# Performance work log

Hardware: AMD Instinct MI355X
Metric: run time of the kernel (lower is better)

The kernel has to match this reference:

```python
import jax, jax.numpy as jnp
import numpy as np
import math

D = 2048
NH = 16       # query heads
NKV = 4       # kv heads (GQA)
HD = 128
SOFTCLAMP = 50.0
ROPE_BASE = 10000.0
B = 4
SQ_VLM = 1024
SQ_ACT = 64
S_CACHE = 256


def _heads(x, n):
    # [B,S,n*HD] -> [B,n,S,HD]
    b, s, _ = x.shape
    return x.reshape(b, s, n, HD).transpose(0, 2, 1, 3)


def _rope_cos_sin(pos):
    # pos: [B,S] int -> cos,sin [B,1,S,HD]
    inv_freq = 1.0 / (ROPE_BASE ** (jnp.arange(0, HD, 2, dtype=jnp.float32) / HD))
    freqs = pos.astype(jnp.float32)[..., None] * inv_freq  # [B,S,HD/2]
    emb = jnp.concatenate([freqs, freqs], axis=-1)         # [B,S,HD]
    return jnp.cos(emb)[:, None], jnp.sin(emb)[:, None]


def _apply_rope(x, cos, sin):
    # x: [B,H,S,HD]
    x1, x2 = x[..., : HD // 2], x[..., HD // 2 :]
    rot = jnp.concatenate([-x2, x1], axis=-1)
    return x * cos + rot * sin


def setup_inputs() -> dict:
    key = jax.random.key(0)
    ks = jax.random.split(key, 16)
    sc = lambda d: 1.0 / math.sqrt(d)
    inp = {
        'attention_mask': jnp.zeros((B, 1, SQ_VLM + SQ_ACT, S_CACHE + SQ_VLM + SQ_ACT), jnp.float32),
        'pos_vlm': jnp.broadcast_to(jnp.arange(S_CACHE, S_CACHE + SQ_VLM, dtype=jnp.int32), (B, SQ_VLM)),
        'pos_action': jnp.broadcast_to(jnp.arange(S_CACHE + SQ_VLM, S_CACHE + SQ_VLM + SQ_ACT, dtype=jnp.int32), (B, SQ_ACT)),
        'h_vlm': jax.random.normal(ks[0], (B, SQ_VLM, D), jnp.float32),
        'h_action': jax.random.normal(ks[1], (B, SQ_ACT, D), jnp.float32),
        'k_cache': jax.random.normal(ks[2], (B, NKV, S_CACHE, HD), jnp.float32),
        'v_cache': jax.random.normal(ks[3], (B, NKV, S_CACHE, HD), jnp.float32),
        'Wq_vlm': jax.random.normal(ks[4], (D, NH * HD), jnp.float32) * sc(D),
        'Wk_vlm': jax.random.normal(ks[5], (D, NKV * HD), jnp.float32) * sc(D),
        'Wv_vlm': jax.random.normal(ks[6], (D, NKV * HD), jnp.float32) * sc(D),
        'Wq_act': jax.random.normal(ks[7], (D, NH * HD), jnp.float32) * sc(D),
        'Wk_act': jax.random.normal(ks[8], (D, NKV * HD), jnp.float32) * sc(D),
        'Wv_act': jax.random.normal(ks[9], (D, NKV * HD), jnp.float32) * sc(D),
        'Wo_act': jax.random.normal(ks[10], (NH * HD, D), jnp.float32) * sc(NH * HD),
    }
    return inp


def reference(attention_mask, pos_vlm, pos_action, h_vlm, h_action, k_cache, v_cache,
              Wq_vlm, Wk_vlm, Wv_vlm, Wq_act, Wk_act, Wv_act, Wo_act):
    group = NH // NKV

    def qkv(h, pos, Wq, Wk, Wv):
        q = _heads(h @ Wq, NH)
        k = _heads(h @ Wk, NKV)
        v = _heads(h @ Wv, NKV)
        cos, sin = _rope_cos_sin(pos)
        return _apply_rope(q, cos, sin), _apply_rope(k, cos, sin), v

    q_v, k_v, v_v = qkv(h_vlm, pos_vlm, Wq_vlm, Wk_vlm, Wv_vlm)
    q_a, k_a, v_a = qkv(h_action, pos_action, Wq_act, Wk_act, Wv_act)

    # repeat_kv (GQA) on every KV source, cached mixture first (append_non_active order)
    rep = lambda t: jnp.repeat(t, group, axis=1)  # [B,NKV,S,HD] -> [B,NH,S,HD]
    k = jnp.concatenate([rep(k_cache), rep(k_v), rep(k_a)], axis=2)
    v = jnp.concatenate([rep(v_cache), rep(v_v), rep(v_a)], axis=2)
    q = jnp.concatenate([q_v, q_a], axis=2)  # [B,NH,Sq,HD]

    scores = jnp.einsum('bhqd,bhkd->bhqk', q, k) / math.sqrt(HD)
    scores = jnp.tanh(scores / SOFTCLAMP) * SOFTCLAMP + attention_mask
    w = jax.nn.softmax(scores.astype(jnp.float32), axis=-1).astype(q.dtype)
    out = jnp.einsum('bhqk,bhkd->bhqd', w, v)
    out = out.transpose(0, 2, 1, 3).reshape(B, SQ_VLM + SQ_ACT, NH * HD)

    # split by q_lens; 'vlm' is in post_attn_skip_names -> no o_proj, dropped
    out_action = out[:, SQ_VLM:, :]
    return out_action @ Wo_act
```

## Files before the change

kernel.cpp:

```cpp
#include <hip/hip_runtime.h>
#include <cmath>

#define NH 16
#define NKV 4
#define HD 128
#define DMODEL 2048
#define BB 4
#define SQV 1024
#define SQA 64
#define SCACHE 256
#define STOT 1344
#define SQTOT 1088
#define NSPLIT 7

typedef unsigned short u16;
typedef __attribute__((ext_vector_type(8))) short short8;
typedef __attribute__((ext_vector_type(4))) float f32x4;

__device__ __forceinline__ float b2f(u16 u) {
    union { float f; unsigned int i; } x; x.i = ((unsigned int)u) << 16; return x.f;
}
__device__ __forceinline__ u16 f2b(float f) {
    unsigned int x = __float_as_uint(f);
    x = x + 0x7fffu + ((x >> 16) & 1u);
    return (u16)(x >> 16);
}

__device__ __forceinline__ void gload16(const void* g, void* l) {
    __builtin_amdgcn_global_load_lds((const __attribute__((address_space(1))) void*)g,
                                     (__attribute__((address_space(3))) void*)l, 16, 0, 0);
}

__device__ __forceinline__ void transpose_body(const float* in, u16* out, int N,
                                               int bx, int by) {
    __shared__ __align__(16) u16 t[64 * 66];
    int n0 = bx * 64, k0 = by * 64;
    int tid = threadIdx.x;
    int r = tid >> 3;
    int c8 = (tid & 7) * 8;
#pragma unroll
    for (int h = 0; h < 2; h++) {
        int k = r + h * 32;
        const float* f = in + (size_t)(k0 + k) * N + n0 + c8;
        float4 a = *(const float4*)f, b = *(const float4*)(f + 4);
        u16 vv[8] = {f2b(a.x), f2b(a.y), f2b(a.z), f2b(a.w),
                     f2b(b.x), f2b(b.y), f2b(b.z), f2b(b.w)};
#pragma unroll
        for (int j = 0; j < 8; j++) t[(c8 + j) * 66 + k] = vv[j];
    }
    __syncthreads();
#pragma unroll
    for (int h = 0; h < 2; h++) {
        int n = r + h * 32;
        short8 v;
#pragma unroll
        for (int j = 0; j < 8; j++) ((u16*)&v)[j] = t[n * 66 + c8 + j];
        *(short8*)(out + (size_t)(n0 + n) * 2048 + k0 + c8) = v;
    }
}

__global__ void k_prep(const float* __restrict__ mask,
                       const float* __restrict__ kc, const float* __restrict__ vc,
                       const float* __restrict__ hv, const float* __restrict__ ha,
                       const float* __restrict__ w0, u16* __restrict__ o0,
                       const float* __restrict__ w1, u16* __restrict__ o1,
                       const float* __restrict__ w2, u16* __restrict__ o2,
                       const float* __restrict__ w3, u16* __restrict__ o3,
                       const float* __restrict__ w4, u16* __restrict__ o4,
                       const float* __restrict__ w5, u16* __restrict__ o5,
                       float* __restrict__ cosT, float* __restrict__ sinT,
                       u16* __restrict__ maskS, u16* __restrict__ K_all, u16* __restrict__ V_all,
                       u16* __restrict__ hv16, u16* __restrict__ ha16) {
    int gx = blockIdx.x, tid = threadIdx.x;
    if (gx < 3072) {
        if (gx < 256)        transpose_body(w0, o0, 512,  gx & 7,  gx >> 3);
        else if (gx < 512)   { int g = gx - 256;  transpose_body(w1, o1, 512,  g & 7,  g >> 3); }
        else if (gx < 768)   { int g = gx - 512;  transpose_body(w2, o2, 512,  g & 7,  g >> 3); }
        else if (gx < 1024)  { int g = gx - 768;  transpose_body(w3, o3, 512,  g & 7,  g >> 3); }
        else if (gx < 2048)  { int g = gx - 1024; transpose_body(w4, o4, 2048, g & 31, g >> 5); }
        else                 { int g = gx - 2048; transpose_body(w5, o5, 2048, g & 31, g >> 5); }
        return;
    }
    int bx = gx - 3072;
    if (bx < 336) {
        int i = bx * 256 + tid;
        if (i < STOT * 64) {
            int p = i >> 6, j = i & 63;
            float inv = __expf(-(float)j * (9.210340371976184f / 64.0f));
            float ang = (float)p * inv;
            cosT[i] = cosf(ang);
            sinT[i] = sinf(ang);
        }
    } else if (bx < 1680) {
        int i = (bx - 336) * 256 + tid;
        int b = i / (SQA * STOT);
        int r = i % (SQA * STOT);
        size_t s = (size_t)b * SQTOT * STOT + (size_t)SQV * STOT + r;
        maskS[i] = f2b(mask[s]);
    } else if (bx < 1936) {
        int i = (bx - 1680) * 256 + tid;
        int e = i * 8;
        int bk = e / (SCACHE * HD);
        int off = e % (SCACHE * HD);
        size_t dst = (size_t)bk * STOT * HD + off;
        const float* fk = kc + e;
        const float* fv = vc + e;
        u16 tk[8], tv[8];
#pragma unroll
        for (int j = 0; j < 8; j++) { tk[j] = f2b(fk[j]); tv[j] = f2b(fv[j]); }
        *(short8*)(K_all + dst) = *(short8*)tk;
        *(short8*)(V_all + dst) = *(short8*)tv;
    } else if (bx < 6032) {
        int i = (bx - 1936) * 256 + tid;
        int e = i * 8;
        const float* f = hv + e;
        float4 a = *(const float4*)f, b = *(const float4*)(f + 4);
        u16 t[8] = {f2b(a.x), f2b(a.y), f2b(a.z), f2b(a.w),
                    f2b(b.x), f2b(b.y), f2b(b.z), f2b(b.w)};
        *(short8*)(hv16 + e) = *(short8*)t;
    } else {
        int i = (bx - 6032) * 256 + tid;
        int e = i * 8;
        const float* f = ha + e;
        float4 a = *(const float4*)f, b = *(const float4*)(f + 4);
        u16 t[8] = {f2b(a.x), f2b(a.y), f2b(a.z), f2b(a.w),
                    f2b(b.x), f2b(b.y), f2b(b.z), f2b(b.w)};
        *(short8*)(ha16 + e) = *(short8*)t;
    }
}

__global__ __launch_bounds__(256) void k_gemm_qkv(
    const u16* __restrict__ Avlm, const u16* __restrict__ Aact,
    const u16* __restrict__ WkvT, const u16* __restrict__ WvvT,
    const u16* __restrict__ WqaT, const u16* __restrict__ WkaT, const u16* __restrict__ WvaT,
    const int* __restrict__ pos_vlm, const int* __restrict__ pos_act,
    const float* __restrict__ cosT, const float* __restrict__ sinT,
    u16* __restrict__ Qbuf, u16* __restrict__ K_all, u16* __restrict__ V_all) {
    __shared__ __align__(16) u16 smem[2 * 12288];
    int tid = threadIdx.x;
    int w = tid >> 6, lane = tid & 63;
    int la = lane & 15, lg = lane >> 4;
    int wm = (w & 1) * 32;
    int c2 = w >> 1;
    int ntab[4] = {c2 * 2, c2 * 2 + 1, c2 * 2 + 4, c2 * 2 + 5};

    const u16* A; const u16* Bt; int m0, n0;
    int path;
    int kv_or_head = 0;
    if (blockIdx.y < 8) {
        int by = blockIdx.y;
        m0 = blockIdx.x * 64;
        A = Avlm;
        path = (by < 4) ? 0 : 1;
        kv_or_head = by & 3;
        n0 = kv_or_head * 128;
        Bt = (path == 0) ? WkvT : WvvT;
    } else {
        int g = (blockIdx.y - 8) * 64 + blockIdx.x;
        if (g >= 96) return;
        m0 = (g & 3) * 64;
        int ny = g >> 2;
        A = Aact;
        if (ny < 16)      { path = 2; kv_or_head = ny;      Bt = WqaT; n0 = ny * 128; }
        else if (ny < 20) { path = 3; kv_or_head = ny - 16; Bt = WkaT; n0 = (ny - 16) * 128; }
        else              { path = 4; kv_or_head = ny - 20; Bt = WvaT; n0 = (ny - 20) * 128; }
    }

    f32x4 acc[2][4];
#pragma unroll
    for (int i = 0; i < 2; i++)
#pragma unroll
        for (int j = 0; j < 4; j++) acc[i][j] = (f32x4){0.f, 0.f, 0.f, 0.f};

    int srow = tid >> 3;
    int scsrc = (((tid & 7) * 16) ^ ((srow & 7) << 4)) >> 1;

#define STAGE_QKV(CB, KB) do {                                                        \
        u16* Ab_ = smem + (CB) * 12288;                                               \
        u16* Bb_ = Ab_ + 4096;                                                        \
        _Pragma("unroll")                                                             \
        for (int h = 0; h < 2; h++)                                                   \
            gload16(A + (size_t)(m0 + srow + h * 32) * DMODEL + (KB) + scsrc,         \
                    Ab_ + h * 2048 + w * 512);                                        \
        _Pragma("unroll")                                                             \
        for (int h = 0; h < 4; h++)                                                   \
            gload16(Bt + (size_t)(n0 + srow + h * 32) * DMODEL + (KB) + scsrc,        \
                    Bb_ + h * 2048 + w * 512);                                        \
    } while (0)

    STAGE_QKV(0, 0);
    int cur = 0;
    int sw = (la & 7) << 3;
    for (int kb = 0; kb < DMODEL; kb += 64) {
        if (kb + 64 < DMODEL) {
            STAGE_QKV(cur ^ 1, kb + 64);
            asm volatile("s_waitcnt vmcnt(6)" ::: "memory");
        } else {
            asm volatile("s_waitcnt vmcnt(0)" ::: "memory");
        }
        __builtin_amdgcn_s_barrier();
        asm volatile("" ::: "memory");
        const u16* Ac = smem + cur * 12288;
        const u16* Bc = Ac + 4096;
#pragma unroll
        for (int kk = 0; kk < 2; kk++) {
            short8 af[2], bf[4];
            int cc = (kk * 32 + lg * 8) ^ sw;
#pragma unroll
            for (int mt = 0; mt < 2; mt++)
                af[mt] = *(const short8*)&Ac[(wm + mt * 16 + la) * 64 + cc];
#pragma unroll
            for (int nt = 0; nt < 4; nt++)
                bf[nt] = *(const short8*)&Bc[(ntab[nt] * 16 + la) * 64 + cc];
#pragma unroll
            for (int mt = 0; mt < 2; mt++)
#pragma unroll
                for (int nt = 0; nt < 4; nt++)
                    acc[mt][nt] = __builtin_amdgcn_mfma_f32_16x16x32_bf16(af[mt], bf[nt], acc[mt][nt], 0, 0, 0);
        }
        __builtin_amdgcn_s_barrier();
        cur ^= 1;
    }
#undef STAGE_QKV

#pragma unroll
    for (int mt = 0; mt < 2; mt++) {
#pragma unroll
        for (int r = 0; r < 4; r++) {
            int gm = m0 + wm + mt * 16 + lg * 4 + r;
            if (path <= 1) {
                int b = gm >> 10, s = gm & 1023;
                size_t base = ((size_t)(b * NKV + kv_or_head) * STOT + SCACHE + s) * HD;
                if (path == 0) {
                    int pos = pos_vlm[gm];
#pragma unroll
                    for (int i = 0; i < 2; i++) {
                        int dlo = ntab[i] * 16 + la;
                        float x1 = acc[mt][i][r], x2 = acc[mt][i + 2][r];
                        float cs = cosT[pos * 64 + dlo], sn = sinT[pos * 64 + dlo];
                        K_all[base + dlo]      = f2b(x1 * cs - x2 * sn);
                        K_all[base + dlo + 64] = f2b(x2 * cs + x1 * sn);
                    }
                } else {
#pragma unroll
                    for (int i = 0; i < 4; i++) V_all[base + ntab[i] * 16 + la] = f2b(acc[mt][i][r]);
                }
            } else {
                int b = gm >> 6, s = gm & 63;
                if (path == 2) {
                    int pos = pos_act[gm];
                    size_t qb = ((size_t)(b * NH + kv_or_head) * SQA + s) * HD;
#pragma unroll
                    for (int i = 0; i < 2; i++) {
                        int dlo = ntab[i] * 16 + la;
                        float x1 = acc[mt][i][r], x2 = acc[mt][i + 2][r];
                        float cs = cosT[pos * 64 + dlo], sn = sinT[pos * 64 + dlo];
                        Qbuf[qb + dlo]      = f2b(x1 * cs - x2 * sn);
                        Qbuf[qb + dlo + 64] = f2b(x2 * cs + x1 * sn);
                    }
                } else if (path == 3) {
                    int pos = pos_act[gm];
                    size_t base = ((size_t)(b * NKV + kv_or_head) * STOT + SCACHE + SQV + s) * HD;
#pragma unroll
                    for (int i = 0; i < 2; i++) {
                        int dlo = ntab[i] * 16 + la;
                        float x1 = acc[mt][i][r], x2 = acc[mt][i + 2][r];
                        float cs = cosT[pos * 64 + dlo], sn = sinT[pos * 64 + dlo];
                        K_all[base + dlo]      = f2b(x1 * cs - x2 * sn);
                        K_all[base + dlo + 64] = f2b(x2 * cs + x1 * sn);
                    }
                } else {
                    size_t base = ((size_t)(b * NKV + kv_or_head) * STOT + SCACHE + SQV + s) * HD;
#pragma unroll
                    for (int i = 0; i < 4; i++) V_all[base + ntab[i] * 16 + la] = f2b(acc[mt][i][r]);
                }
            }
        }
    }
}

__global__ __launch_bounds__(256) void k_attn_split(
    const u16* __restrict__ Qbuf, const u16* __restrict__ K_all, const u16* __restrict__ V_all,
    const u16* __restrict__ maskS, u16* __restrict__ po, float* __restrict__ pml) {
    int h = blockIdx.x, b = blockIdx.y, p = blockIdx.z;
    int bh = b * NH + h;
    int kvh = h >> 2;
    const u16* Kb = K_all + (size_t)(b * NKV + kvh) * STOT * HD;
    const u16* Vb = V_all + (size_t)(b * NKV + kvh) * STOT * HD;
    const u16* Qb = Qbuf + (size_t)bh * SQA * HD;
    int tid = threadIdx.x, w = tid >> 6, lane = tid & 63;
    int la = lane & 15, lg = lane >> 4;
    __shared__ __align__(16) u16 Ks[64 * 136];
    __shared__ __align__(16) u16 Vs[64 * 130];
    __shared__ __align__(16) u16 Ps[4][16 * 72];
    short8 qf[4];
#pragma unroll
    for (int kk = 0; kk < 4; kk++)
        qf[kk] = *(const short8*)(Qb + (size_t)(w * 16 + la) * HD + kk * 32 + lg * 8);
    f32x4 o_acc[8];
#pragma unroll
    for (int nt = 0; nt < 8; nt++) o_acc[nt] = (f32x4){0.f, 0.f, 0.f, 0.f};
    float m_run[4], l_run[4];
#pragma unroll
    for (int r = 0; r < 4; r++) { m_run[r] = -3e38f; l_run[r] = 0.f; }
    int vr = tid >> 4;
    int vc = (tid & 15) * 8;
    const float scl = 0.08838834764831845f;
    for (int c = 0; c < 3; c++) {
        int g = p * 3 + c;
#pragma unroll
        for (int hh = 0; hh < 4; hh++) {
            int key = vr + hh * 16;
            *(short8*)&Ks[key * 136 + vc] = *(const short8*)(Kb + (size_t)(g * 64 + key) * HD + vc);
            short8 vv = *(const short8*)(Vb + (size_t)(g * 64 + key) * HD + vc);
            unsigned int* d32 = (unsigned int*)&Vs[key * 130 + vc];
#pragma unroll
            for (int q2 = 0; q2 < 4; q2++) d32[q2] = ((unsigned int*)&vv)[q2];
        }
        __syncthreads();
        f32x4 s_acc[4];
#pragma unroll
        for (int nt = 0; nt < 4; nt++) s_acc[nt] = (f32x4){0.f, 0.f, 0.f, 0.f};
#pragma unroll
        for (int kk = 0; kk < 4; kk++) {
#pragma unroll
            for (int nt = 0; nt < 4; nt++) {
                short8 kf = *(const short8*)&Ks[(nt * 16 + la) * 136 + kk * 32 + lg * 8];
                s_acc[nt] = __builtin_amdgcn_mfma_f32_16x16x32_bf16(qf[kk], kf, s_acc[nt], 0, 0, 0);
            }
        }
        float sc[4][4];
#pragma unroll
        for (int nt = 0; nt < 4; nt++) {
            int key = g * 64 + nt * 16 + la;
#pragma unroll
            for (int r = 0; r < 4; r++) {
                int sq = w * 16 + lg * 4 + r;
                float sv = s_acc[nt][r] * scl;
                float x = sv * 0.02f;
                float t = __expf(-2.0f * fabsf(x));
                float th = __fdividef(1.0f - t, 1.0f + t);
                sv = copysignf(th, x) * 50.0f;
                sv += b2f(maskS[((size_t)(b * SQA + sq)) * STOT + key]);
                sc[nt][r] = sv;
            }
        }
#pragma unroll
        for (int r = 0; r < 4; r++) {
            float mx = fmaxf(fmaxf(sc[0][r], sc[1][r]), fmaxf(sc[2][r], sc[3][r]));
#pragma unroll
            for (int sh = 1; sh < 16; sh <<= 1) mx = fmaxf(mx, __shfl_xor(mx, sh, 64));
            float mn = fmaxf(m_run[r], mx);
            float alpha = __expf(m_run[r] - mn);
            m_run[r] = mn;
            float rowsum = 0.f;
#pragma unroll
            for (int nt = 0; nt < 4; nt++) {
                float pv = __expf(sc[nt][r] - mn);
                Ps[w][(lg * 4 + r) * 72 + nt * 16 + la] = f2b(pv);
                rowsum += pv;
            }
#pragma unroll
            for (int sh = 1; sh < 16; sh <<= 1) rowsum += __shfl_xor(rowsum, sh, 64);
            l_run[r] = l_run[r] * alpha + rowsum;
#pragma unroll
            for (int nt = 0; nt < 8; nt++) o_acc[nt][r] *= alpha;
        }
        __syncthreads();
#pragma unroll
        for (int kk = 0; kk < 2; kk++) {
            short8 pf = *(const short8*)&Ps[w][la * 72 + kk * 32 + lg * 8];
#pragma unroll
            for (int nt = 0; nt < 8; nt++) {
                short8 vf;
#pragma unroll
                for (int j = 0; j < 8; j++) ((u16*)&vf)[j] = Vs[(kk * 32 + lg * 8 + j) * 130 + nt * 16 + la];
                o_acc[nt] = __builtin_amdgcn_mfma_f32_16x16x32_bf16(pf, vf, o_acc[nt], 0, 0, 0);
            }
        }
        __syncthreads();
    }
#pragma unroll
    for (int nt = 0; nt < 8; nt++) {
#pragma unroll
        for (int r = 0; r < 4; r++) {
            int sq = w * 16 + lg * 4 + r;
            po[(((size_t)p * 64 + bh) * 64 + sq) * 128 + nt * 16 + la] = f2b(o_acc[nt][r]);
        }
    }
    if (la == 0) {
#pragma unroll
        for (int r = 0; r < 4; r++) {
            int sq = w * 16 + lg * 4 + r;
            size_t mlb = (((size_t)p * 64 + bh) * 64 + sq) * 2;
            pml[mlb] = m_run[r];
            pml[mlb + 1] = l_run[r];
        }
    }
}

__global__ __launch_bounds__(256) void k_attn_red(
    const u16* __restrict__ po, const float* __restrict__ pml, u16* __restrict__ AO) {
    int h = blockIdx.x, b = blockIdx.y;
    int bh = b * NH + h;
    __shared__ float wgt[NSPLIT][64];
    int tid = threadIdx.x;
    if (tid < 64) {
        int q = tid;
        float m[NSPLIT], l[NSPLIT], M = -3e38f;
#pragma unroll
        for (int p = 0; p < NSPLIT; p++) {
            size_t mlb = (((size_t)p * 64 + bh) * 64 + q) * 2;
            m[p] = pml[mlb]; l[p] = pml[mlb + 1];
            M = fmaxf(M, m[p]);
        }
        float L = 0.f;
#pragma unroll
        for (int p = 0; p < NSPLIT; p++) L += l[p] * __expf(m[p] - M);
        float inv = 1.0f / L;
#pragma unroll
        for (int p = 0; p < NSPLIT; p++) wgt[p][q] = __expf(m[p] - M) * inv;
    }
    __syncthreads();
    for (int e = tid; e < 64 * 128; e += 256) {
        int q = e >> 7, d = e & 127;
        float s = 0.f;
#pragma unroll
        for (int p = 0; p < NSPLIT; p++)
            s += b2f(po[(((size_t)p * 64 + bh) * 64 + q) * 128 + d]) * wgt[p][q];
        AO[((size_t)(b * SQA + q)) * 2048 + h * HD + d] = f2b(s);
    }
}

__global__ __launch_bounds__(256) void k_gemm_out(
    const u16* __restrict__ A, const u16* __restrict__ WoT, float* __restrict__ out) {
    __shared__ __align__(16) u16 smem[2 * 8192];
    int m0 = blockIdx.x * 64, n0 = blockIdx.y * 64;
    int tid = threadIdx.x;
    int w = tid >> 6, lane = tid & 63;
    int la = lane & 15, lg = lane >> 4;
    int wm = (w & 1) * 32, wn = (w >> 1) * 32;
    f32x4 acc[2][2];
#pragma unroll
    for (int i = 0; i < 2; i++)
#pragma unroll
        for (int j = 0; j < 2; j++) acc[i][j] = (f32x4){0.f, 0.f, 0.f, 0.f};

    int srow = tid >> 3;
    int scsrc = (((tid & 7) * 16) ^ ((srow & 7) << 4)) >> 1;

#define STAGE_OUT(CB, KB) do {                                                        \
        u16* Ab_ = smem + (CB) * 8192;                                                \
        u16* Bb_ = Ab_ + 4096;                                                        \
        _Pragma("unroll")                                                             \
        for (int h = 0; h < 2; h++)                                                   \
            gload16(A + (size_t)(m0 + srow + h * 32) * DMODEL + (KB) + scsrc,         \
                    Ab_ + h * 2048 + w * 512);                                        \
        _Pragma("unroll")                                                             \
        for (int h = 0; h < 2; h++)                                                   \
            gload16(WoT + (size_t)(n0 + srow + h * 32) * DMODEL + (KB) + scsrc,       \
                    Bb_ + h * 2048 + w * 512);                                        \
    } while (0)

    STAGE_OUT(0, 0);
    int cur = 0;
    int sw = (la & 7) << 3;
    for (int kb = 0; kb < DMODEL; kb += 64) {
        if (kb + 64 < DMODEL) {
            STAGE_OUT(cur ^ 1, kb + 64);
            asm volatile("s_waitcnt vmcnt(4)" ::: "memory");
        } else {
            asm volatile("s_waitcnt vmcnt(0)" ::: "memory");
        }
        __builtin_amdgcn_s_barrier();
        asm volatile("" ::: "memory");
        const u16* Ac = smem + cur * 8192;
        const u16* Bc = Ac + 4096;
#pragma unroll
        for (int kk = 0; kk < 2; kk++) {
            short8 af[2], bf[2];
            int cc = (kk * 32 + lg * 8) ^ sw;
#pragma unroll
            for (int mt = 0; mt < 2; mt++) af[mt] = *(const short8*)&Ac[(wm + mt * 16 + la) * 64 + cc];
#pragma unroll
            for (int nt = 0; nt < 2; nt++) bf[nt] = *(const short8*)&Bc[(wn + nt * 16 + la) * 64 + cc];
#pragma unroll
            for (int mt = 0; mt < 2; mt++)
#pragma unroll
                for (int nt = 0; nt < 2; nt++)
                    acc[mt][nt] = __builtin_amdgcn_mfma_f32_16x16x32_bf16(af[mt], bf[nt], acc[mt][nt], 0, 0, 0);
        }
        __builtin_amdgcn_s_barrier();
        cur ^= 1;
    }
#undef STAGE_OUT

#pragma unroll
    for (int mt = 0; mt < 2; mt++) {
#pragma unroll
        for (int r = 0; r < 4; r++) {
            int gm = m0 + wm + mt * 16 + lg * 4 + r;
#pragma unroll
            for (int nt = 0; nt < 2; nt++)
                out[(size_t)gm * DMODEL + n0 + wn + nt * 16 + la] = acc[mt][nt][r];
        }
    }
}

extern "C" void kernel_launch(void* const* d_in, const int* in_sizes, int n_in,
                              void* d_out, int out_size, void* d_ws, size_t ws_size,
                              hipStream_t stream) {
    (void)in_sizes; (void)n_in; (void)out_size;
    const float* mask    = (const float*)d_in[0];
    const int*   pos_vlm = (const int*)d_in[1];
    const int*   pos_act = (const int*)d_in[2];
    const float* h_vlm   = (const float*)d_in[3];
    const float* h_act   = (const float*)d_in[4];
    const float* k_cache = (const float*)d_in[5];
    const float* v_cache = (const float*)d_in[6];
    const float* Wk_vlm  = (const float*)d_in[8];
    const float* Wv_vlm  = (const float*)d_in[9];
    const float* Wq_act  = (const float*)d_in[10];
    const float* Wk_act  = (const float*)d_in[11];
    const float* Wv_act  = (const float*)d_in[12];
    const float* Wo_act  = (const float*)d_in[13];

    const size_t NEED = 65273856;
    if (ws_size < NEED) return;
    char* ws = (char*)d_ws;
    float* cosT  = (float*)(ws + 0);
    float* sinT  = (float*)(ws + 344064);
    u16* K_all   = (u16*)(ws + 688128);
    u16* V_all   = (u16*)(ws + 6193152);
    u16* Qbuf    = (u16*)(ws + 11698176);
    u16* AO      = (u16*)(ws + 12746752);
    u16* WkvT    = (u16*)(ws + 13795328);
    u16* WvvT    = (u16*)(ws + 15892480);
    u16* WqaT    = (u16*)(ws + 17989632);
    u16* WkaT    = (u16*)(ws + 26378240);
    u16* WvaT    = (u16*)(ws + 28475392);
    u16* WoT     = (u16*)(ws + 30572544);
    u16* po      = (u16*)(ws + 38961152);
    float* pml   = (float*)(ws + 46301184);
    u16* maskS   = (u16*)(ws + 46759936);
    u16* hv16    = (u16*)(ws + 47448064);
    u16* ha16    = (u16*)(ws + 64225280);

    hipLaunchKernelGGL(k_prep, dim3(9360), dim3(256), 0, stream,
                       mask, k_cache, v_cache, h_vlm, h_act,
                       Wk_vlm, WkvT, Wv_vlm, WvvT, Wk_act, WkaT, Wv_act, WvaT,
                       Wq_act, WqaT, Wo_act, WoT,
                       cosT, sinT, maskS, K_all, V_all, hv16, ha16);
    hipLaunchKernelGGL(k_gemm_qkv, dim3(64, 10), dim3(256), 0, stream,
                       hv16, ha16, WkvT, WvvT, WqaT, WkaT, WvaT,
                       pos_vlm, pos_act, cosT, sinT, Qbuf, K_all, V_all);
    hipLaunchKernelGGL(k_attn_split, dim3(16, 4, NSPLIT), dim3(256), 0, stream,
                       Qbuf, K_all, V_all, maskS, po, pml);
    hipLaunchKernelGGL(k_attn_red, dim3(16, 4), dim3(256), 0, stream, po, pml, AO);
    hipLaunchKernelGGL(k_gemm_out, dim3(4, 32), dim3(256), 0, stream, AO, WoT, (float*)d_out);
}
```

Measured before the change: 239.1 us.

## Store V transposed, double-buffer attention K/V loads, enlarge QKV GEMM tiles

V is now stored transposed ([d][key]) by both the prep kernel and the QKV GEMM epilogue. This lets the attention kernel load V fragments as contiguous short8 reads instead of gathering them element by element. The attention loop now double-buffers K/V tiles into swizzled shared memory with async global loads, preloads the mask into registers, and raises wave priority around the MFMA sections. The QKV GEMM moves to 128x128 tiles on a 1D grid of 304 blocks, which uses more LDS and registers per block and makes the transposed V epilogue stores strided.

```diff
diff --git a/kernel.cpp b/kernel.cpp
--- a/kernel.cpp
+++ b/kernel.cpp
@@ -59,6 +59,35 @@
     }
 }
 
+__device__ __forceinline__ void transpose_vc(const float* vc, u16* VT, int idx) {
+    __shared__ __align__(16) u16 tv[64 * 66];
+    int bkv = idx >> 3, t8 = idx & 7;
+    int key0 = (t8 >> 1) * 64, d0 = (t8 & 1) * 64;
+    const float* in = vc + ((size_t)bkv * SCACHE + key0) * HD + d0;
+    u16* out = VT + ((size_t)bkv * HD + d0) * STOT + key0;
+    int tid = threadIdx.x;
+    int r = tid >> 3, c8 = (tid & 7) * 8;
+#pragma unroll
+    for (int h = 0; h < 2; h++) {
+        int k = r + h * 32;
+        const float* f = in + (size_t)k * HD + c8;
+        float4 a = *(const float4*)f, b = *(const float4*)(f + 4);
+        u16 vv[8] = {f2b(a.x), f2b(a.y), f2b(a.z), f2b(a.w),
+                     f2b(b.x), f2b(b.y), f2b(b.z), f2b(b.w)};
+#pragma unroll
+        for (int j = 0; j < 8; j++) tv[(c8 + j) * 66 + k] = vv[j];
+    }
+    __syncthreads();
+#pragma unroll
+    for (int h = 0; h < 2; h++) {
+        int d = r + h * 32;
+        short8 v;
+#pragma unroll
+        for (int j = 0; j < 8; j++) ((u16*)&v)[j] = tv[d * 66 + c8 + j];
+        *(short8*)(out + (size_t)d * STOT + c8) = v;
+    }
+}
+
 __global__ void k_prep(const float* __restrict__ mask,
                        const float* __restrict__ kc, const float* __restrict__ vc,
                        const float* __restrict__ hv, const float* __restrict__ ha,
@@ -69,7 +98,7 @@
                        const float* __restrict__ w4, u16* __restrict__ o4,
                        const float* __restrict__ w5, u16* __restrict__ o5,
                        float* __restrict__ cosT, float* __restrict__ sinT,
-                       u16* __restrict__ maskS, u16* __restrict__ K_all, u16* __restrict__ V_all,
+                       u16* __restrict__ maskS, u16* __restrict__ K_all, u16* __restrict__ VT_all,
                        u16* __restrict__ hv16, u16* __restrict__ ha16) {
     int gx = blockIdx.x, tid = threadIdx.x;
     if (gx < 3072) {
@@ -104,12 +133,10 @@
         int off = e % (SCACHE * HD);
         size_t dst = (size_t)bk * STOT * HD + off;
         const float* fk = kc + e;
-        const float* fv = vc + e;
-        u16 tk[8], tv[8];
-#pragma unroll
-        for (int j = 0; j < 8; j++) { tk[j] = f2b(fk[j]); tv[j] = f2b(fv[j]); }
+        u16 tk[8];
+#pragma unroll
+        for (int j = 0; j < 8; j++) tk[j] = f2b(fk[j]);
         *(short8*)(K_all + dst) = *(short8*)tk;
-        *(short8*)(V_all + dst) = *(short8*)tv;
     } else if (bx < 6032) {
         int i = (bx - 1936) * 256 + tid;
         int e = i * 8;
@@ -118,7 +145,7 @@
         u16 t[8] = {f2b(a.x), f2b(a.y), f2b(a.z), f2b(a.w),
                     f2b(b.x), f2b(b.y), f2b(b.z), f2b(b.w)};
         *(short8*)(hv16 + e) = *(short8*)t;
-    } else {
+    } else if (bx < 6288) {
         int i = (bx - 6032) * 256 + tid;
         int e = i * 8;
         const float* f = ha + e;
@@ -126,6 +153,8 @@
         u16 t[8] = {f2b(a.x), f2b(a.y), f2b(a.z), f2b(a.w),
                     f2b(b.x), f2b(b.y), f2b(b.z), f2b(b.w)};
         *(short8*)(ha16 + e) = *(short8*)t;
+    } else {
+        transpose_vc(vc, VT_all, bx - 6288);
     }
 }
 
@@ -135,40 +164,40 @@
     const u16* __restrict__ WqaT, const u16* __restrict__ WkaT, const u16* __restrict__ WvaT,
     const int* __restrict__ pos_vlm, const int* __restrict__ pos_act,
     const float* __restrict__ cosT, const float* __restrict__ sinT,
-    u16* __restrict__ Qbuf, u16* __restrict__ K_all, u16* __restrict__ V_all) {
-    __shared__ __align__(16) u16 smem[2 * 12288];
+    u16* __restrict__ Qbuf, u16* __restrict__ K_all, u16* __restrict__ VT_all) {
+    __shared__ __align__(16) u16 smem[2 * 16384];
     int tid = threadIdx.x;
     int w = tid >> 6, lane = tid & 63;
     int la = lane & 15, lg = lane >> 4;
-    int wm = (w & 1) * 32;
+    int wm = (w & 1) * 64;
     int c2 = w >> 1;
     int ntab[4] = {c2 * 2, c2 * 2 + 1, c2 * 2 + 4, c2 * 2 + 5};
 
     const u16* A; const u16* Bt; int m0, n0;
     int path;
-    int kv_or_head = 0;
-    if (blockIdx.y < 8) {
-        int by = blockIdx.y;
-        m0 = blockIdx.x * 64;
+    int head;
+    int bid = blockIdx.x;
+    if (bid < 256) {
+        m0 = (bid & 31) * 128;
+        int yy = bid >> 5;
+        path = (yy < 4) ? 0 : 1;
+        head = yy & 3;
+        n0 = head * 128;
         A = Avlm;
-        path = (by < 4) ? 0 : 1;
-        kv_or_head = by & 3;
-        n0 = kv_or_head * 128;
         Bt = (path == 0) ? WkvT : WvvT;
     } else {
-        int g = (blockIdx.y - 8) * 64 + blockIdx.x;
-        if (g >= 96) return;
-        m0 = (g & 3) * 64;
-        int ny = g >> 2;
+        int g = bid - 256;
+        m0 = (g & 1) * 128;
+        int ny = g >> 1;
         A = Aact;
-        if (ny < 16)      { path = 2; kv_or_head = ny;      Bt = WqaT; n0 = ny * 128; }
-        else if (ny < 20) { path = 3; kv_or_head = ny - 16; Bt = WkaT; n0 = (ny - 16) * 128; }
-        else              { path = 4; kv_or_head = ny - 20; Bt = WvaT; n0 = (ny - 20) * 128; }
-    }
-
-    f32x4 acc[2][4];
-#pragma unroll
-    for (int i = 0; i < 2; i++)
+        if (ny < 16)      { path = 2; head = ny;      Bt = WqaT; n0 = ny * 128; }
+        else if (ny < 20) { path = 3; head = ny - 16; Bt = WkaT; n0 = (ny - 16) * 128; }
+        else              { path = 4; head = ny - 20; Bt = WvaT; n0 = (ny - 20) * 128; }
+    }
+
+    f32x4 acc[4][4];
+#pragma unroll
+    for (int i = 0; i < 4; i++)
 #pragma unroll
         for (int j = 0; j < 4; j++) acc[i][j] = (f32x4){0.f, 0.f, 0.f, 0.f};
 
@@ -176,44 +205,44 @@
     int scsrc = (((tid & 7) * 16) ^ ((srow & 7) << 4)) >> 1;
 
 #define STAGE_QKV(CB, KB) do {                                                        \
-        u16* Ab_ = smem + (CB) * 12288;                                               \
-        u16* Bb_ = Ab_ + 4096;                                                        \
+        u16* Ab_ = smem + (CB) * 16384;                                               \
+        u16* Bb_ = Ab_ + 8192;                                                        \
         _Pragma("unroll")                                                             \
-        for (int h = 0; h < 2; h++)                                                   \
+        for (int h = 0; h < 4; h++)                                                   \
             gload16(A + (size_t)(m0 + srow + h * 32) * DMODEL + (KB) + scsrc,         \
-                    Ab_ + h * 2048 + w * 512);                                        \
+                    Ab_ + h * 2048 + tid * 8);                                        \
         _Pragma("unroll")                                                             \
         for (int h = 0; h < 4; h++)                                                   \
             gload16(Bt + (size_t)(n0 + srow + h * 32) * DMODEL + (KB) + scsrc,        \
-                    Bb_ + h * 2048 + w * 512);                                        \
+                    Bb_ + h * 2048 + tid * 8);                                        \
     } while (0)
 
     STAGE_QKV(0, 0);
     int cur = 0;
-    int sw = (la & 7) << 3;
+    int swr = (la & 7) << 3;
     for (int kb = 0; kb < DMODEL; kb += 64) {
         if (kb + 64 < DMODEL) {
             STAGE_QKV(cur ^ 1, kb + 64);
-            asm volatile("s_waitcnt vmcnt(6)" ::: "memory");
+            asm volatile("s_waitcnt vmcnt(8)" ::: "memory");
         } else {
             asm volatile("s_waitcnt vmcnt(0)" ::: "memory");
         }
         __builtin_amdgcn_s_barrier();
         asm volatile("" ::: "memory");
-        const u16* Ac = smem + cur * 12288;
-        const u16* Bc = Ac + 4096;
+        const u16* Ac = smem + cur * 16384;
+        const u16* Bc = Ac + 8192;
 #pragma unroll
         for (int kk = 0; kk < 2; kk++) {
-            short8 af[2], bf[4];
-            int cc = (kk * 32 + lg * 8) ^ sw;
-#pragma unroll
-            for (int mt = 0; mt < 2; mt++)
+            short8 af[4], bf[4];
+            int cc = (kk * 32 + lg * 8) ^ swr;
+#pragma unroll
+            for (int mt = 0; mt < 4; mt++)
                 af[mt] = *(const short8*)&Ac[(wm + mt * 16 + la) * 64 + cc];
 #pragma unroll
             for (int nt = 0; nt < 4; nt++)
                 bf[nt] = *(const short8*)&Bc[(ntab[nt] * 16 + la) * 64 + cc];
 #pragma unroll
-            for (int mt = 0; mt < 2; mt++)
+            for (int mt = 0; mt < 4; mt++)
 #pragma unroll
                 for (int nt = 0; nt < 4; nt++)
                     acc[mt][nt] = __builtin_amdgcn_mfma_f32_16x16x32_bf16(af[mt], bf[nt], acc[mt][nt], 0, 0, 0);
@@ -224,14 +253,14 @@
 #undef STAGE_QKV
 
 #pragma unroll
-    for (int mt = 0; mt < 2; mt++) {
+    for (int mt = 0; mt < 4; mt++) {
 #pragma unroll
         for (int r = 0; r < 4; r++) {
             int gm = m0 + wm + mt * 16 + lg * 4 + r;
             if (path <= 1) {
                 int b = gm >> 10, s = gm & 1023;
-                size_t base = ((size_t)(b * NKV + kv_or_head) * STOT + SCACHE + s) * HD;
                 if (path == 0) {
+                    size_t base = ((size_t)(b * NKV + head) * STOT + SCACHE + s) * HD;
                     int pos = pos_vlm[gm];
 #pragma unroll
                     for (int i = 0; i < 2; i++) {
@@ -242,14 +271,18 @@
                         K_all[base + dlo + 64] = f2b(x2 * cs + x1 * sn);
                     }
                 } else {
-#pragma unroll
-                    for (int i = 0; i < 4; i++) V_all[base + ntab[i] * 16 + la] = f2b(acc[mt][i][r]);
+                    size_t vt = ((size_t)(b * NKV + head) * HD) * STOT + SCACHE + s;
+#pragma unroll
+                    for (int i = 0; i < 4; i++) {
+                        int d = ntab[i] * 16 + la;
+                        VT_all[vt + (size_t)d * STOT] = f2b(acc[mt][i][r]);
+                    }
                 }
             } else {
                 int b = gm >> 6, s = gm & 63;
                 if (path == 2) {
                     int pos = pos_act[gm];
-                    size_t qb = ((size_t)(b * NH + kv_or_head) * SQA + s) * HD;
+                    size_t qb = ((size_t)(b * NH + head) * SQA + s) * HD;
 #pragma unroll
                     for (int i = 0; i < 2; i++) {
                         int dlo = ntab[i] * 16 + la;
@@ -260,7 +293,7 @@
                     }
                 } else if (path == 3) {
                     int pos = pos_act[gm];
-                    size_t base = ((size_t)(b * NKV + kv_or_head) * STOT + SCACHE + SQV + s) * HD;
+                    size_t base = ((size_t)(b * NKV + head) * STOT + SCACHE + SQV + s) * HD;
 #pragma unroll
                     for (int i = 0; i < 2; i++) {
                         int dlo = ntab[i] * 16 + la;
@@ -270,9 +303,12 @@
                         K_all[base + dlo + 64] = f2b(x2 * cs + x1 * sn);
                     }
                 } else {
-                    size_t base = ((size_t)(b * NKV + kv_or_head) * STOT + SCACHE + SQV + s) * HD;
-#pragma unroll
-                    for (int i = 0; i < 4; i++) V_all[base + ntab[i] * 16 + la] = f2b(acc[mt][i][r]);
+                    size_t vt = ((size_t)(b * NKV + head) * HD) * STOT + SCACHE + SQV + s;
+#pragma unroll
+                    for (int i = 0; i < 4; i++) {
+                        int d = ntab[i] * 16 + la;
+                        VT_all[vt + (size_t)d * STOT] = f2b(acc[mt][i][r]);
+                    }
                 }
             }
         }
@@ -280,18 +316,18 @@
 }
 
 __global__ __launch_bounds__(256) void k_attn_split(
-    const u16* __restrict__ Qbuf, const u16* __restrict__ K_all, const u16* __restrict__ V_all,
+    const u16* __restrict__ Qbuf, const u16* __restrict__ K_all, const u16* __restrict__ VT_all,
     const u16* __restrict__ maskS, u16* __restrict__ po, float* __restrict__ pml) {
     int h = blockIdx.x, b = blockIdx.y, p = blockIdx.z;
     int bh = b * NH + h;
     int kvh = h >> 2;
-    const u16* Kb = K_all + (size_t)(b * NKV + kvh) * STOT * HD;
-    const u16* Vb = V_all + (size_t)(b * NKV + kvh) * STOT * HD;
-    const u16* Qb = Qbuf + (size_t)bh * SQA * HD;
+    const u16* Kb  = K_all  + (size_t)(b * NKV + kvh) * STOT * HD;
+    const u16* VTb = VT_all + (size_t)(b * NKV + kvh) * HD * STOT;
+    const u16* Qb  = Qbuf + (size_t)bh * SQA * HD;
     int tid = threadIdx.x, w = tid >> 6, lane = tid & 63;
     int la = lane & 15, lg = lane >> 4;
-    __shared__ __align__(16) u16 Ks[64 * 136];
-    __shared__ __align__(16) u16 Vs[64 * 130];
+    __shared__ __align__(16) u16 Ks[2][64 * 128];
+    __shared__ __align__(16) u16 Vt[2][128 * 64];
     __shared__ __align__(16) u16 Ps[4][16 * 72];
     short8 qf[4];
 #pragma unroll
@@ -303,45 +339,69 @@
     float m_run[4], l_run[4];
 #pragma unroll
     for (int r = 0; r < 4; r++) { m_run[r] = -3e38f; l_run[r] = 0.f; }
-    int vr = tid >> 4;
-    int vc = (tid & 15) * 8;
+
+    int kr = tid >> 4;
+    int ksw = (((tid & 15) * 16) ^ ((kr & 7) << 4)) >> 1;
+    int vr = tid >> 3;
+    int vsw = (((tid & 7) * 16) ^ ((vr & 7) << 4)) >> 1;
+
+#define ASTAGE(CB, G) do {                                                            \
+        _Pragma("unroll")                                                             \
+        for (int hh = 0; hh < 4; hh++)                                                \
+            gload16(Kb + (size_t)((G) * 64 + kr + hh * 16) * HD + ksw,                \
+                    &Ks[CB][hh * 2048 + tid * 8]);                                    \
+        _Pragma("unroll")                                                             \
+        for (int hh = 0; hh < 4; hh++)                                                \
+            gload16(VTb + (size_t)(vr + hh * 32) * STOT + (G) * 64 + vsw,             \
+                    &Vt[CB][hh * 2048 + tid * 8]);                                    \
+    } while (0)
+
+    ASTAGE(0, p * 3);
+    int cur = 0;
+    int swr = (la & 7) << 3;
     const float scl = 0.08838834764831845f;
     for (int c = 0; c < 3; c++) {
         int g = p * 3 + c;
-#pragma unroll
-        for (int hh = 0; hh < 4; hh++) {
-            int key = vr + hh * 16;
-            *(short8*)&Ks[key * 136 + vc] = *(const short8*)(Kb + (size_t)(g * 64 + key) * HD + vc);
-            short8 vv = *(const short8*)(Vb + (size_t)(g * 64 + key) * HD + vc);
-            unsigned int* d32 = (unsigned int*)&Vs[key * 130 + vc];
-#pragma unroll
-            for (int q2 = 0; q2 < 4; q2++) d32[q2] = ((unsigned int*)&vv)[q2];
-        }
-        __syncthreads();
+        u16 mreg[4][4];
+#pragma unroll
+        for (int nt = 0; nt < 4; nt++)
+#pragma unroll
+            for (int r = 0; r < 4; r++)
+                mreg[nt][r] = maskS[((size_t)(b * SQA + w * 16 + lg * 4 + r)) * STOT +
+                                    g * 64 + nt * 16 + la];
+        if (c < 2) {
+            ASTAGE(cur ^ 1, g + 1);
+            asm volatile("s_waitcnt vmcnt(8)" ::: "memory");
+        } else {
+            asm volatile("s_waitcnt vmcnt(0)" ::: "memory");
+        }
+        __builtin_amdgcn_s_barrier();
+        asm volatile("" ::: "memory");
         f32x4 s_acc[4];
 #pragma unroll
         for (int nt = 0; nt < 4; nt++) s_acc[nt] = (f32x4){0.f, 0.f, 0.f, 0.f};
+        __builtin_amdgcn_s_setprio(1);
 #pragma unroll
         for (int kk = 0; kk < 4; kk++) {
+            int cc = (kk * 32 + lg * 8) ^ swr;
 #pragma unroll
             for (int nt = 0; nt < 4; nt++) {
-                short8 kf = *(const short8*)&Ks[(nt * 16 + la) * 136 + kk * 32 + lg * 8];
+                short8 kf = *(const short8*)&Ks[cur][(nt * 16 + la) * 128 + cc];
                 s_acc[nt] = __builtin_amdgcn_mfma_f32_16x16x32_bf16(qf[kk], kf, s_acc[nt], 0, 0, 0);
             }
         }
+        __builtin_amdgcn_s_setprio(0);
         float sc[4][4];
 #pragma unroll
         for (int nt = 0; nt < 4; nt++) {
-            int key = g * 64 + nt * 16 + la;
 #pragma unroll
             for (int r = 0; r < 4; r++) {
-                int sq = w * 16 + lg * 4 + r;
                 float sv = s_acc[nt][r] * scl;
                 float x = sv * 0.02f;
                 float t = __expf(-2.0f * fabsf(x));
                 float th = __fdividef(1.0f - t, 1.0f + t);
                 sv = copysignf(th, x) * 50.0f;
-                sv += b2f(maskS[((size_t)(b * SQA + sq)) * STOT + key]);
+                sv += b2f(mreg[nt][r]);
                 sc[nt][r] = sv;
             }
         }
@@ -366,20 +426,22 @@
 #pragma unroll
             for (int nt = 0; nt < 8; nt++) o_acc[nt][r] *= alpha;
         }
-        __syncthreads();
+        __builtin_amdgcn_s_setprio(1);
 #pragma unroll
         for (int kk = 0; kk < 2; kk++) {
             short8 pf = *(const short8*)&Ps[w][la * 72 + kk * 32 + lg * 8];
+            int cc = (kk * 32 + lg * 8) ^ swr;
 #pragma unroll
             for (int nt = 0; nt < 8; nt++) {
-                short8 vf;
-#pragma unroll
-                for (int j = 0; j < 8; j++) ((u16*)&vf)[j] = Vs[(kk * 32 + lg * 8 + j) * 130 + nt * 16 + la];
+                short8 vf = *(const short8*)&Vt[cur][(nt * 16 + la) * 64 + cc];
                 o_acc[nt] = __builtin_amdgcn_mfma_f32_16x16x32_bf16(pf, vf, o_acc[nt], 0, 0, 0);
             }
         }
-        __syncthreads();
-    }
+        __builtin_amdgcn_s_setprio(0);
+        __builtin_amdgcn_s_barrier();
+        cur ^= 1;
+    }
+#undef ASTAGE
 #pragma unroll
     for (int nt = 0; nt < 8; nt++) {
 #pragma unroll
@@ -464,7 +526,7 @@
 
     STAGE_OUT(0, 0);
     int cur = 0;
-    int sw = (la & 7) << 3;
+    int swr = (la & 7) << 3;
     for (int kb = 0; kb < DMODEL; kb += 64) {
         if (kb + 64 < DMODEL) {
             STAGE_OUT(cur ^ 1, kb + 64);
@@ -479,7 +541,7 @@
 #pragma unroll
         for (int kk = 0; kk < 2; kk++) {
             short8 af[2], bf[2];
-            int cc = (kk * 32 + lg * 8) ^ sw;
+            int cc = (kk * 32 + lg * 8) ^ swr;
 #pragma unroll
             for (int mt = 0; mt < 2; mt++) af[mt] = *(const short8*)&Ac[(wm + mt * 16 + la) * 64 + cc];
 #pragma unroll
@@ -531,7 +593,7 @@
     float* cosT  = (float*)(ws + 0);
     float* sinT  = (float*)(ws + 344064);
     u16* K_all   = (u16*)(ws + 688128);
-    u16* V_all   = (u16*)(ws + 6193152);
+    u16* VT_all  = (u16*)(ws + 6193152);
     u16* Qbuf    = (u16*)(ws + 11698176);
     u16* AO      = (u16*)(ws + 12746752);
     u16* WkvT    = (u16*)(ws + 13795328);
@@ -546,16 +608,16 @@
     u16* hv16    = (u16*)(ws + 47448064);
     u16* ha16    = (u16*)(ws + 64225280);
 
-    hipLaunchKernelGGL(k_prep, dim3(9360), dim3(256), 0, stream,
+    hipLaunchKernelGGL(k_prep, dim3(9488), dim3(256), 0, stream,
                        mask, k_cache, v_cache, h_vlm, h_act,
                        Wk_vlm, WkvT, Wv_vlm, WvvT, Wk_act, WkaT, Wv_act, WvaT,
                        Wq_act, WqaT, Wo_act, WoT,
-                       cosT, sinT, maskS, K_all, V_all, hv16, ha16);
-    hipLaunchKernelGGL(k_gemm_qkv, dim3(64, 10), dim3(256), 0, stream,
+                       cosT, sinT, maskS, K_all, VT_all, hv16, ha16);
+    hipLaunchKernelGGL(k_gemm_qkv, dim3(304), dim3(256), 0, stream,
                        hv16, ha16, WkvT, WvvT, WqaT, WkaT, WvaT,
-                       pos_vlm, pos_act, cosT, sinT, Qbuf, K_all, V_all);
+                       pos_vlm, pos_act, cosT, sinT, Qbuf, K_all, VT_all);
     hipLaunchKernelGGL(k_attn_split, dim3(16, 4, NSPLIT), dim3(256), 0, stream,
-                       Qbuf, K_all, V_all, maskS, po, pml);
+                       Qbuf, K_all, VT_all, maskS, po, pml);
     hipLaunchKernelGGL(k_attn_red, dim3(16, 4), dim3(256), 0, stream, po, pml, AO);
     hipLaunchKernelGGL(k_gemm_out, dim3(4, 32), dim3(256), 0, stream, AO, WoT, (float*)d_out);
 }
```

New measurement: 233.6 us. -2.3%, faster.
